# Kernel tuning notes

Hardware: AMD Instinct MI355X
Metric: run time of the kernel (lower is better)

The kernel has to match this reference:

```python
import jax, jax.numpy as jnp
import numpy as np

EMBED = 1024
D_FF = 4 * EMBED
N_EXPERTS = 8
TOP_K = 2
B, S = 2, 1024


def setup_inputs() -> dict:
    key = jax.random.key(0)
    ks = jax.random.split(key, 10)
    sc_d = 1.0 / np.sqrt(EMBED)
    sc_h = 1.0 / np.sqrt(D_FF)
    return {
        "inputs": jax.random.normal(ks[0], (B, S, EMBED), jnp.float32),
        # router MLP: Linear(D,4D) -> ReLU -> Linear(4D,E)
        "rw1": jax.random.normal(ks[1], (EMBED, D_FF), jnp.float32) * sc_d,
        "rb1": jnp.zeros((D_FF,), jnp.float32),
        "rw2": jax.random.normal(ks[2], (D_FF, N_EXPERTS), jnp.float32) * sc_h,
        "rb2": jnp.zeros((N_EXPERTS,), jnp.float32),
        # stacked expert weights: Linear(D,4D) -> ReLU -> Linear(4D,D)
        "W1": jax.random.normal(ks[3], (N_EXPERTS, EMBED, D_FF), jnp.float32) * sc_d,
        "b1": jnp.zeros((N_EXPERTS, D_FF), jnp.float32),
        "W2": jax.random.normal(ks[4], (N_EXPERTS, D_FF, EMBED), jnp.float32) * sc_h,
        "b2": jnp.zeros((N_EXPERTS, EMBED), jnp.float32),
    }


def reference(inputs, rw1, rb1, rw2, rb2, W1, b1, W2, b2):
    Bb, Ss, D = inputs.shape
    T = Bb * Ss
    xf = inputs.reshape(T, D)  # [T, D]

    # Router: scores over experts, keep top-k, softmax over kept entries only.
    score = jax.nn.relu(xf @ rw1 + rb1) @ rw2 + rb2          # [T, E]
    _, topi = jax.lax.top_k(score, TOP_K)                    # [T, K]
    mask = jnp.zeros(score.shape, bool).at[jnp.arange(T)[:, None], topi].set(True)
    gate = jax.nn.softmax(jnp.where(mask, score, -jnp.inf), axis=-1)  # [T, E]

    # Dense per-expert MLP weighted by gate; gate==0 for non-top-k experts,
    # matching the original masked gather/scatter exactly.
    out = jnp.zeros_like(xf)
    for e in range(N_EXPERTS):
        h = jax.nn.relu(xf @ W1[e] + b1[e])                  # [T, 4D]
        y = h @ W2[e] + b2[e]                                # [T, D]
        out = out + gate[:, e:e + 1] * y
    return out.reshape(Bb, Ss, D)
```

## Files before the change

kernel.cpp:

```cpp
#include <hip/hip_runtime.h>
#include <stdint.h>

typedef unsigned short ushort_t;
typedef __attribute__((ext_vector_type(8))) short short8;
typedef __attribute__((ext_vector_type(4))) float f32x4;

#define EMBED   1024
#define DFF     4096
#define NEXP    8
#define TOKENS  2048
#define SLOTS   4096
#define TMAX    40

__device__ __forceinline__ ushort_t f2bf(float f) {
  unsigned u = __float_as_uint(f);
  u += 0x7FFFu + ((u >> 16) & 1u);
  return (ushort_t)(u >> 16);
}
__device__ __forceinline__ float bf2f(ushort_t b) {
  return __uint_as_float(((unsigned)b) << 16);
}

__device__ __forceinline__ void gl2lds16(const void* g, void* l) {
  typedef const __attribute__((address_space(1))) unsigned char* gp_t;
  typedef __attribute__((address_space(3))) unsigned char* lp_t;
  __builtin_amdgcn_global_load_lds((gp_t)(uintptr_t)g, (lp_t)(uintptr_t)l, 16, 0, 0);
}

__global__ void zero_small(int* counts, int* cursors) {
  int i = threadIdx.x;
  if (i < NEXP) { counts[i] = 0; cursors[i] = 0; }
}

__global__ void split_x3(const float* __restrict__ x, ushort_t* __restrict__ Xs) {
  int t = blockIdx.x;
  int d = threadIdx.x * 4;
  float4 v = *(const float4*)(x + (size_t)t * EMBED + d);
  ushort4 hi, lo;
  hi.x = f2bf(v.x); lo.x = f2bf(v.x - bf2f(hi.x));
  hi.y = f2bf(v.y); lo.y = f2bf(v.y - bf2f(hi.y));
  hi.z = f2bf(v.z); lo.z = f2bf(v.z - bf2f(hi.z));
  hi.w = f2bf(v.w); lo.w = f2bf(v.w - bf2f(hi.w));
  ushort_t* row = Xs + (size_t)t * 3072;
  *(ushort4*)(row + d)        = hi;
  *(ushort4*)(row + 1024 + d) = lo;
  *(ushort4*)(row + 2048 + d) = hi;
}

__global__ void transp_conv(const float* __restrict__ src, ushort_t* __restrict__ dst,
                            int src_ld, int dst_ld, long src_estride, long dst_estride,
                            int dst_koff, int lo)
{
  __shared__ float t[64][65];
  const float* s = src + (size_t)blockIdx.z * src_estride;
  ushort_t* d = dst + (size_t)blockIdx.z * dst_estride;
  int n0 = blockIdx.x * 64, k0 = blockIdx.y * 64;
  int tid = threadIdx.x;
  int kk = tid >> 4, nn = (tid & 15) * 4;
  #pragma unroll
  for (int it = 0; it < 4; it++) {
    float4 v = *(const float4*)(s + (size_t)(k0 + kk + it * 16) * src_ld + n0 + nn);
    t[kk + it * 16][nn]     = v.x;
    t[kk + it * 16][nn + 1] = v.y;
    t[kk + it * 16][nn + 2] = v.z;
    t[kk + it * 16][nn + 3] = v.w;
  }
  __syncthreads();
  int nn2 = tid >> 3, kk2 = (tid & 7) * 8;
  #pragma unroll
  for (int it = 0; it < 2; it++) {
    int n = nn2 + it * 32;
    union { ushort_t u[8]; uint4 v; } pk;
    #pragma unroll
    for (int j = 0; j < 8; j++) {
      float xv = t[kk2 + j][n];
      ushort_t hv = f2bf(xv);
      pk.u[j] = lo ? f2bf(xv - bf2f(hv)) : hv;
    }
    *(uint4*)(d + (size_t)(n0 + n) * dst_ld + dst_koff + k0 + kk2) = pk.v;
  }
}

template<int BPATH, int OUTMODE, bool RELU, bool EXPERT, int SPLITK, int NX>
__global__ __launch_bounds__(256, 4)
void gemm_kernel(const ushort_t* __restrict__ A, const void* __restrict__ Bv,
                 const float* __restrict__ bias, void* __restrict__ Cout,
                 const float* __restrict__ slot_gate, const int* __restrict__ slot_token,
                 const int* __restrict__ off, const int* __restrict__ tile_e,
                 const int* __restrict__ tile_y, int M, int N, int K)
{
  __shared__ ushort_t As[128 * 32];
  __shared__ ushort_t Bs[128 * 32];

  int e = 0, kc = 0, row0, col0, m_base, m_cnt;
  if (EXPERT) {
    int bid  = blockIdx.x;
    int xi   = bid % NX;
    int rest = bid / NX;
    kc       = rest % SPLITK;
    int t    = rest / SPLITK;
    e = tile_e[t];
    if (e < 0) return;
    row0   = tile_y[t] * 128;
    col0   = xi * 128;
    m_base = off[e];
    m_cnt  = off[e + 1] - m_base;
  } else {
    row0 = blockIdx.y * 128;
    col0 = blockIdx.x * 128;
    m_base = 0; m_cnt = M;
    if (row0 >= m_cnt) return;
  }
  const int Kc   = K / SPLITK;
  const int kbeg = kc * Kc;

  const int tid  = threadIdx.x;
  const int lane = tid & 63;
  const int wid  = tid >> 6;
  const int wm = wid & 1, wn = wid >> 1;

  const int srow  = lane >> 2;
  const int schk8 = ((lane & 3) ^ ((lane >> 3) & 3)) * 8;

  const ushort_t* gA[2];
  ushort_t *ldsA[2], *ldsB[2];
  #pragma unroll
  for (int h = 0; h < 2; h++) {
    int r  = row0 + h * 64 + wid * 16 + srow;
    int rg = m_base + min(r, m_cnt - 1);
    gA[h]   = A + (size_t)rg * K + kbeg + schk8;
    ldsA[h] = As + (h * 64 + wid * 16) * 32;
    ldsB[h] = Bs + (h * 64 + wid * 16) * 32;
  }
  const ushort_t* gB[2] = {nullptr, nullptr};
  const float* Bf = nullptr;
  if constexpr (BPATH == 0) {
    const ushort_t* Bt = (const ushort_t*)Bv + (EXPERT ? (size_t)e * N * K : 0);
    #pragma unroll
    for (int h = 0; h < 2; h++) {
      int n = col0 + h * 64 + wid * 16 + srow;
      gB[h] = Bt + (size_t)n * K + kbeg + schk8;
    }
  } else {
    Bf = (const float*)Bv + (EXPERT ? (size_t)e * (size_t)K * N : 0);
  }
  const int bn  = tid & 127;
  const int bc0 = (tid >> 7) << 1;

  f32x4 acc[4][4];
  #pragma unroll
  for (int i = 0; i < 4; i++)
    #pragma unroll
    for (int j = 0; j < 4; j++)
      acc[i][j] = (f32x4){0.f, 0.f, 0.f, 0.f};

  const int q  = lane >> 4;
  const int rr = lane & 15;
  const int sw8 = (q ^ ((rr >> 1) & 3)) * 8;
  const int abase = (wm * 64 + rr) * 32 + sw8;
  const int bbase = (wn * 64 + rr) * 32 + sw8;

  const int nkt = Kc >> 5;
  for (int kt = 0; kt < nkt; kt++) {
    const int k0 = kt << 5;
    __syncthreads();
    #pragma unroll
    for (int h = 0; h < 2; h++) gl2lds16(gA[h] + k0, ldsA[h]);
    if constexpr (BPATH == 0) {
      #pragma unroll
      for (int h = 0; h < 2; h++) gl2lds16(gB[h] + k0, ldsB[h]);
    } else {
      #pragma unroll
      for (int ci = 0; ci < 2; ci++) {
        int c = bc0 + ci;
        union { ushort_t u[8]; uint4 v; } pk;
        #pragma unroll
        for (int j = 0; j < 8; j++)
          pk.u[j] = f2bf(Bf[(size_t)(kbeg + k0 + c * 8 + j) * N + col0 + bn]);
        int s = c ^ ((bn >> 1) & 3);
        *(uint4*)(Bs + bn * 32 + s * 8) = pk.v;
      }
    }
    __syncthreads();

    short8 af[4], bfr[4];
    #pragma unroll
    for (int i = 0; i < 4; i++) {
      af[i]  = *(const short8*)(As + abase + i * 512);
      bfr[i] = *(const short8*)(Bs + bbase + i * 512);
    }
    #pragma unroll
    for (int mt = 0; mt < 4; mt++)
      #pragma unroll
      for (int nt = 0; nt < 4; nt++)
        acc[mt][nt] = __builtin_amdgcn_mfma_f32_16x16x32_bf16(af[mt], bfr[nt], acc[mt][nt], 0, 0, 0);
  }

  const float* biasp = bias + (EXPERT ? (size_t)e * N : 0);
  float bv[4];
  #pragma unroll
  for (int nt = 0; nt < 4; nt++)
    bv[nt] = biasp[col0 + wn * 64 + nt * 16 + rr];
  const float bscale = (SPLITK == 1 || kc == 0) ? 1.f : 0.f;

  #pragma unroll
  for (int mt = 0; mt < 4; mt++) {
    #pragma unroll
    for (int i = 0; i < 4; i++) {
      int r_loc = row0 + wm * 64 + mt * 16 + q * 4 + i;
      if (r_loc < m_cnt) {
        int slot = m_base + r_loc;
        float g = 1.f; int tok = 0;
        if (OUTMODE == 2) { g = slot_gate[slot]; tok = slot_token[slot]; }
        #pragma unroll
        for (int nt = 0; nt < 4; nt++) {
          float v = acc[mt][nt][i] + bscale * bv[nt];
          if (RELU) v = fmaxf(v, 0.f);
          int c = col0 + wn * 64 + nt * 16 + rr;
          if (OUTMODE == 0)      ((float*)Cout)[(size_t)slot * N + c]    = v;
          else if (OUTMODE == 1) ((ushort_t*)Cout)[(size_t)slot * N + c] = f2bf(v);
          else atomicAdd(&((float*)Cout)[(size_t)tok * N + c], g * v);
        }
      }
    }
  }
}

__global__ void router_score(const float* __restrict__ h, const float* __restrict__ rw2,
                             const float* __restrict__ rb2, int* __restrict__ topi,
                             float* __restrict__ gates, int* __restrict__ counts)
{
  int t = blockIdx.x * 4 + (threadIdx.x >> 6);
  if (t >= TOKENS) return;
  int lane = threadIdx.x & 63;
  const float* hr = h + (size_t)t * DFF;
  float acc[8] = {0,0,0,0,0,0,0,0};
  for (int j = lane; j < DFF; j += 64) {
    float hv = hr[j];
    const float4* w = (const float4*)(rw2 + (size_t)j * 8);
    float4 w0 = w[0], w1 = w[1];
    acc[0] += hv * w0.x; acc[1] += hv * w0.y; acc[2] += hv * w0.z; acc[3] += hv * w0.w;
    acc[4] += hv * w1.x; acc[5] += hv * w1.y; acc[6] += hv * w1.z; acc[7] += hv * w1.w;
  }
  #pragma unroll
  for (int e = 0; e < 8; e++)
    for (int o = 32; o > 0; o >>= 1)
      acc[e] += __shfl_down(acc[e], o);
  if (lane == 0) {
    float s[8];
    #pragma unroll
    for (int e = 0; e < 8; e++) s[e] = acc[e] + rb2[e];
    int i0 = 0;
    #pragma unroll
    for (int e = 1; e < 8; e++) if (s[e] > s[i0]) i0 = e;
    int i1 = (i0 == 0) ? 1 : 0;
    #pragma unroll
    for (int e = 0; e < 8; e++) if (e != i0 && s[e] > s[i1]) i1 = e;
    float ex = __expf(s[i1] - s[i0]);
    float g0 = 1.f / (1.f + ex);
    float g1 = ex / (1.f + ex);
    topi[t * 2] = i0; topi[t * 2 + 1] = i1;
    gates[t * 2] = g0; gates[t * 2 + 1] = g1;
    atomicAdd(&counts[i0], 1);
    atomicAdd(&counts[i1], 1);
  }
}

__global__ void prefix_off(const int* __restrict__ counts, int* __restrict__ off,
                           int* __restrict__ tile_e, int* __restrict__ tile_y)
{
  if (threadIdx.x == 0) {
    int a = 0, t = 0;
    for (int e = 0; e < NEXP; e++) {
      off[e] = a;
      int c = counts[e]; a += c;
      int ty = (c + 127) >> 7;
      for (int y = 0; y < ty; y++) { tile_e[t] = e; tile_y[t] = y; t++; }
    }
    off[NEXP] = a;
    for (; t < TMAX; t++) { tile_e[t] = -1; tile_y[t] = 0; }
  }
}

__global__ void assign_slots(const int* __restrict__ topi, const float* __restrict__ gates,
                             const int* __restrict__ off, int* __restrict__ cursors,
                             int* __restrict__ slot_token, float* __restrict__ slot_gate)
{
  int t = blockIdx.x * blockDim.x + threadIdx.x;
  if (t >= TOKENS) return;
  #pragma unroll
  for (int k = 0; k < 2; k++) {
    int e = topi[t * 2 + k];
    int p = atomicAdd(&cursors[e], 1);
    int s = off[e] + p;
    slot_token[s] = t;
    slot_gate[s]  = gates[t * 2 + k];
  }
}

__global__ void gather_x(const float* __restrict__ x, const int* __restrict__ slot_token,
                         ushort_t* __restrict__ Xg)
{
  int s = blockIdx.x;
  int t = slot_token[s];
  int d = threadIdx.x * 4;
  float4 v = *(const float4*)(x + (size_t)t * EMBED + d);
  ushort4 o;
  o.x = f2bf(v.x); o.y = f2bf(v.y); o.z = f2bf(v.z); o.w = f2bf(v.w);
  *(ushort4*)(Xg + (size_t)s * EMBED + d) = o;
}

extern "C" void kernel_launch(void* const* d_in, const int* in_sizes, int n_in,
                              void* d_out, int out_size, void* d_ws, size_t ws_size,
                              hipStream_t stream)
{
  const float* x   = (const float*)d_in[0];
  const float* rw1 = (const float*)d_in[1];
  const float* rb1 = (const float*)d_in[2];
  const float* rw2 = (const float*)d_in[3];
  const float* rb2 = (const float*)d_in[4];
  const float* W1  = (const float*)d_in[5];
  const float* b1  = (const float*)d_in[6];
  const float* W2  = (const float*)d_in[7];
  const float* b2  = (const float*)d_in[8];
  float* out = (float*)d_out;
  char* ws = (char*)d_ws;

  const size_t SZ_RW1T = (size_t)4096 * 3072 * 2;
  const size_t SZ_XS3  = (size_t)2048 * 3072 * 2;
  const size_t SZ_WT   = (size_t)NEXP * 4096 * 1024 * 2;
  const size_t SZ_XG   = (size_t)SLOTS * EMBED * 2;
  const size_t SZ_H    = (size_t)SLOTS * DFF * 2;
  const size_t SZ_SMALL = 131072;
  const size_t NEED_A  = SZ_WT + SZ_XG + SZ_H + SZ_SMALL;
  const bool layoutA = (ws_size >= NEED_A);

  ushort_t *RW1t, *Xs3, *Wt, *Xg, *Hs;
  char* ps;
  if (layoutA) {
    Wt   = (ushort_t*)ws;
    RW1t = (ushort_t*)ws;
    Xs3  = (ushort_t*)(ws + SZ_RW1T);
    Xg   = (ushort_t*)(ws + SZ_WT);
    Hs   = (ushort_t*)(ws + SZ_WT + SZ_XG);
    ps   = ws + SZ_WT + SZ_XG + SZ_H;
  } else {
    Wt   = nullptr;
    RW1t = (ushort_t*)ws;
    Xs3  = (ushort_t*)(ws + SZ_RW1T);
    Xg   = (ushort_t*)(ws + SZ_RW1T + SZ_XS3);
    Hs   = (ushort_t*)(ws + SZ_RW1T + SZ_XS3 + SZ_XG);
    ps   = ws + SZ_RW1T + SZ_XS3 + SZ_XG + SZ_H;
  }
  float* h = (float*)Hs;
  int*   topi       = (int*)ps;    ps += TOKENS * 2 * 4;
  float* gates      = (float*)ps;  ps += TOKENS * 2 * 4;
  int*   slot_token = (int*)ps;    ps += SLOTS * 4;
  float* slot_gate  = (float*)ps;  ps += SLOTS * 4;
  int*   counts     = (int*)ps;    ps += 256;
  int*   cursors    = (int*)ps;    ps += 256;
  int*   off        = (int*)ps;    ps += 256;
  int*   tile_e     = (int*)ps;    ps += 256;
  int*   tile_y     = (int*)ps;    ps += 256;

  hipMemsetAsync(d_out, 0, (size_t)TOKENS * EMBED * 4, stream);
  zero_small<<<1, 64, 0, stream>>>(counts, cursors);
  split_x3<<<TOKENS, 256, 0, stream>>>(x, Xs3);

  transp_conv<<<dim3(64, 16, 1), 256, 0, stream>>>(rw1, RW1t, DFF, 3072, 0, 0, 0,    0);
  transp_conv<<<dim3(64, 16, 1), 256, 0, stream>>>(rw1, RW1t, DFF, 3072, 0, 0, 1024, 0);
  transp_conv<<<dim3(64, 16, 1), 256, 0, stream>>>(rw1, RW1t, DFF, 3072, 0, 0, 2048, 1);

  gemm_kernel<0, 0, true, false, 1, 32>
      <<<dim3(32, 16, 1), 256, 0, stream>>>(Xs3, RW1t, rb1, h, nullptr, nullptr,
                                            nullptr, nullptr, nullptr, TOKENS, DFF, 3072);
  router_score<<<512, 256, 0, stream>>>(h, rw2, rb2, topi, gates, counts);
  prefix_off  <<<1, 64, 0, stream>>>(counts, off, tile_e, tile_y);
  assign_slots<<<8, 256, 0, stream>>>(topi, gates, off, cursors, slot_token, slot_gate);
  gather_x    <<<SLOTS, 256, 0, stream>>>(x, slot_token, Xg);

  if (layoutA) {
    transp_conv<<<dim3(64, 16, NEXP), 256, 0, stream>>>(
        W1, Wt, DFF, EMBED, (long)EMBED * DFF, (long)DFF * EMBED, 0, 0);
    gemm_kernel<0, 1, true, true, 1, 32>
        <<<dim3(32 * TMAX, 1, 1), 256, 0, stream>>>(Xg, Wt, b1, Hs,
            nullptr, nullptr, off, tile_e, tile_y, 0, DFF, EMBED);
    transp_conv<<<dim3(16, 64, NEXP), 256, 0, stream>>>(
        W2, Wt, EMBED, DFF, (long)DFF * EMBED, (long)EMBED * DFF, 0, 0);
    gemm_kernel<0, 2, false, true, 4, 8>
        <<<dim3(8 * 4 * TMAX, 1, 1), 256, 0, stream>>>(Hs, Wt, b2, out,
            slot_gate, slot_token, off, tile_e, tile_y, 0, EMBED, DFF);
  } else {
    gemm_kernel<1, 1, true, true, 1, 32>
        <<<dim3(32 * TMAX, 1, 1), 256, 0, stream>>>(Xg, W1, b1, Hs,
            nullptr, nullptr, off, tile_e, tile_y, 0, DFF, EMBED);
    gemm_kernel<1, 2, false, true, 4, 8>
        <<<dim3(8 * 4 * TMAX, 1, 1), 256, 0, stream>>>(Hs, W2, b2, out,
            slot_gate, slot_token, off, tile_e, tile_y, 0, EMBED, DFF);
  }
}
```

Baseline: 671.1 us.

## Replace atomic scatter with split-K partial buffers and deterministic combine kernel

```diff
diff --git a/kernel.cpp b/kernel.cpp
--- a/kernel.cpp
+++ b/kernel.cpp
@@ -85,7 +85,7 @@
 __global__ __launch_bounds__(256, 4)
 void gemm_kernel(const ushort_t* __restrict__ A, const void* __restrict__ Bv,
                  const float* __restrict__ bias, void* __restrict__ Cout,
-                 const float* __restrict__ slot_gate, const int* __restrict__ slot_token,
+                 const float* __restrict__ slot_gate,
                  const int* __restrict__ off, const int* __restrict__ tile_e,
                  const int* __restrict__ tile_y, int M, int N, int K)
 {
@@ -210,8 +210,8 @@
       int r_loc = row0 + wm * 64 + mt * 16 + q * 4 + i;
       if (r_loc < m_cnt) {
         int slot = m_base + r_loc;
-        float g = 1.f; int tok = 0;
-        if (OUTMODE == 2) { g = slot_gate[slot]; tok = slot_token[slot]; }
+        float g = 1.f;
+        if (OUTMODE == 3) g = slot_gate[slot];
         #pragma unroll
         for (int nt = 0; nt < 4; nt++) {
           float v = acc[mt][nt][i] + bscale * bv[nt];
@@ -219,7 +219,7 @@
           int c = col0 + wn * 64 + nt * 16 + rr;
           if (OUTMODE == 0)      ((float*)Cout)[(size_t)slot * N + c]    = v;
           else if (OUTMODE == 1) ((ushort_t*)Cout)[(size_t)slot * N + c] = f2bf(v);
-          else atomicAdd(&((float*)Cout)[(size_t)tok * N + c], g * v);
+          else ((float*)Cout)[((size_t)kc * SLOTS + slot) * N + c] = g * v;
         }
       }
     }
@@ -284,7 +284,8 @@
 
 __global__ void assign_slots(const int* __restrict__ topi, const float* __restrict__ gates,
                              const int* __restrict__ off, int* __restrict__ cursors,
-                             int* __restrict__ slot_token, float* __restrict__ slot_gate)
+                             int* __restrict__ slot_token, float* __restrict__ slot_gate,
+                             int* __restrict__ tok_slot)
 {
   int t = blockIdx.x * blockDim.x + threadIdx.x;
   if (t >= TOKENS) return;
@@ -295,6 +296,7 @@
     int s = off[e] + p;
     slot_token[s] = t;
     slot_gate[s]  = gates[t * 2 + k];
+    tok_slot[t * 2 + k] = s;
   }
 }
 
@@ -308,6 +310,24 @@
   ushort4 o;
   o.x = f2bf(v.x); o.y = f2bf(v.y); o.z = f2bf(v.z); o.w = f2bf(v.w);
   *(ushort4*)(Xg + (size_t)s * EMBED + d) = o;
+}
+
+__global__ void combine_out(const float* __restrict__ Ys, const int* __restrict__ tok_slot,
+                            float* __restrict__ out)
+{
+  int t = blockIdx.x;
+  int d = threadIdx.x * 4;
+  int s0 = tok_slot[t * 2], s1 = tok_slot[t * 2 + 1];
+  float4 a = *(const float4*)(Ys + (size_t)s0 * EMBED + d);
+  float4 b = *(const float4*)(Ys + ((size_t)SLOTS + s0) * EMBED + d);
+  float4 c = *(const float4*)(Ys + (size_t)s1 * EMBED + d);
+  float4 e = *(const float4*)(Ys + ((size_t)SLOTS + s1) * EMBED + d);
+  float4 o;
+  o.x = (a.x + b.x) + (c.x + e.x);
+  o.y = (a.y + b.y) + (c.y + e.y);
+  o.z = (a.z + b.z) + (c.z + e.z);
+  o.w = (a.w + b.w) + (c.w + e.w);
+  *(float4*)(out + (size_t)t * EMBED + d) = o;
 }
 
 extern "C" void kernel_launch(void* const* d_in, const int* in_sizes, int n_in,
@@ -328,33 +348,19 @@
 
   const size_t SZ_RW1T = (size_t)4096 * 3072 * 2;
   const size_t SZ_XS3  = (size_t)2048 * 3072 * 2;
-  const size_t SZ_WT   = (size_t)NEXP * 4096 * 1024 * 2;
   const size_t SZ_XG   = (size_t)SLOTS * EMBED * 2;
   const size_t SZ_H    = (size_t)SLOTS * DFF * 2;
-  const size_t SZ_SMALL = 131072;
-  const size_t NEED_A  = SZ_WT + SZ_XG + SZ_H + SZ_SMALL;
-  const bool layoutA = (ws_size >= NEED_A);
-
-  ushort_t *RW1t, *Xs3, *Wt, *Xg, *Hs;
-  char* ps;
-  if (layoutA) {
-    Wt   = (ushort_t*)ws;
-    RW1t = (ushort_t*)ws;
-    Xs3  = (ushort_t*)(ws + SZ_RW1T);
-    Xg   = (ushort_t*)(ws + SZ_WT);
-    Hs   = (ushort_t*)(ws + SZ_WT + SZ_XG);
-    ps   = ws + SZ_WT + SZ_XG + SZ_H;
-  } else {
-    Wt   = nullptr;
-    RW1t = (ushort_t*)ws;
-    Xs3  = (ushort_t*)(ws + SZ_RW1T);
-    Xg   = (ushort_t*)(ws + SZ_RW1T + SZ_XS3);
-    Hs   = (ushort_t*)(ws + SZ_RW1T + SZ_XS3 + SZ_XG);
-    ps   = ws + SZ_RW1T + SZ_XS3 + SZ_XG + SZ_H;
-  }
-  float* h = (float*)Hs;
+
+  ushort_t* RW1t = (ushort_t*)ws;
+  float*    Ys   = (float*)ws;
+  ushort_t* Xs3  = (ushort_t*)(ws + SZ_RW1T);
+  ushort_t* Xg   = (ushort_t*)(ws + SZ_RW1T + SZ_XS3);
+  ushort_t* Hs   = (ushort_t*)(ws + SZ_RW1T + SZ_XS3 + SZ_XG);
+  float*    h    = (float*)Hs;
+  char* ps = ws + SZ_RW1T + SZ_XS3 + SZ_XG + SZ_H;
   int*   topi       = (int*)ps;    ps += TOKENS * 2 * 4;
   float* gates      = (float*)ps;  ps += TOKENS * 2 * 4;
+  int*   tok_slot   = (int*)ps;    ps += TOKENS * 2 * 4;
   int*   slot_token = (int*)ps;    ps += SLOTS * 4;
   float* slot_gate  = (float*)ps;  ps += SLOTS * 4;
   int*   counts     = (int*)ps;    ps += 256;
@@ -363,7 +369,6 @@
   int*   tile_e     = (int*)ps;    ps += 256;
   int*   tile_y     = (int*)ps;    ps += 256;
 
-  hipMemsetAsync(d_out, 0, (size_t)TOKENS * EMBED * 4, stream);
   zero_small<<<1, 64, 0, stream>>>(counts, cursors);
   split_x3<<<TOKENS, 256, 0, stream>>>(x, Xs3);
 
@@ -372,30 +377,19 @@
   transp_conv<<<dim3(64, 16, 1), 256, 0, stream>>>(rw1, RW1t, DFF, 3072, 0, 0, 2048, 1);
 
   gemm_kernel<0, 0, true, false, 1, 32>
-      <<<dim3(32, 16, 1), 256, 0, stream>>>(Xs3, RW1t, rb1, h, nullptr, nullptr,
+      <<<dim3(32, 16, 1), 256, 0, stream>>>(Xs3, RW1t, rb1, h, nullptr,
                                             nullptr, nullptr, nullptr, TOKENS, DFF, 3072);
   router_score<<<512, 256, 0, stream>>>(h, rw2, rb2, topi, gates, counts);
   prefix_off  <<<1, 64, 0, stream>>>(counts, off, tile_e, tile_y);
-  assign_slots<<<8, 256, 0, stream>>>(topi, gates, off, cursors, slot_token, slot_gate);
+  assign_slots<<<8, 256, 0, stream>>>(topi, gates, off, cursors, slot_token, slot_gate, tok_slot);
   gather_x    <<<SLOTS, 256, 0, stream>>>(x, slot_token, Xg);
 
-  if (layoutA) {
-    transp_conv<<<dim3(64, 16, NEXP), 256, 0, stream>>>(
-        W1, Wt, DFF, EMBED, (long)EMBED * DFF, (long)DFF * EMBED, 0, 0);
-    gemm_kernel<0, 1, true, true, 1, 32>
-        <<<dim3(32 * TMAX, 1, 1), 256, 0, stream>>>(Xg, Wt, b1, Hs,
-            nullptr, nullptr, off, tile_e, tile_y, 0, DFF, EMBED);
-    transp_conv<<<dim3(16, 64, NEXP), 256, 0, stream>>>(
-        W2, Wt, EMBED, DFF, (long)DFF * EMBED, (long)EMBED * DFF, 0, 0);
-    gemm_kernel<0, 2, false, true, 4, 8>
-        <<<dim3(8 * 4 * TMAX, 1, 1), 256, 0, stream>>>(Hs, Wt, b2, out,
-            slot_gate, slot_token, off, tile_e, tile_y, 0, EMBED, DFF);
-  } else {
-    gemm_kernel<1, 1, true, true, 1, 32>
-        <<<dim3(32 * TMAX, 1, 1), 256, 0, stream>>>(Xg, W1, b1, Hs,
-            nullptr, nullptr, off, tile_e, tile_y, 0, DFF, EMBED);
-    gemm_kernel<1, 2, false, true, 4, 8>
-        <<<dim3(8 * 4 * TMAX, 1, 1), 256, 0, stream>>>(Hs, W2, b2, out,
-            slot_gate, slot_token, off, tile_e, tile_y, 0, EMBED, DFF);
-  }
-}
+  gemm_kernel<1, 1, true, true, 1, 32>
+      <<<dim3(32 * TMAX, 1, 1), 256, 0, stream>>>(Xg, W1, b1, Hs,
+          nullptr, off, tile_e, tile_y, 0, DFF, EMBED);
+  gemm_kernel<1, 3, false, true, 2, 8>
+      <<<dim3(8 * 2 * TMAX, 1, 1), 256, 0, stream>>>(Hs, W2, b2, Ys,
+          slot_gate, off, tile_e, tile_y, 0, EMBED, DFF);
+
+  combine_out<<<TOKENS, 256, 0, stream>>>(Ys, tok_slot, out);
+}
```

Result: faster. 625.7 us (-6.8%).
